# Optimization experiments

Measured on AMD Instinct MI355X. Metric: run time of the kernel, lower is better.

## Reference

```python
import jax, jax.numpy as jnp
import numpy as np

N, C_IN, T, V = 64, 64, 256, 25
C_OUT, S, MAX_N = 256, 3, 500
BN_EPS = 1e-5


def setup_inputs() -> dict:
    key = jax.random.key(0)
    ks = jax.random.split(key, 7)
    x = jax.random.normal(ks[0], (N, C_IN, T, V), dtype=jnp.float32)
    A = jax.random.uniform(ks[1], (S, V, V), dtype=jnp.float32) / V  # fixed adjacency (non-trainable buffer)
    A_pers = jax.random.normal(ks[2], (MAX_N, S, V, V), dtype=jnp.float32) * 1e-3
    # conv_branch_init: std = sqrt(2/(out*1*1*branches))
    conv_w = jax.random.normal(ks[3], (S, C_OUT, C_IN), dtype=jnp.float32) * np.sqrt(2.0 / (C_OUT * S)).astype(np.float32)
    conv_b = jax.random.normal(ks[4], (S, C_OUT), dtype=jnp.float32) * 0.01
    bn_w = jax.random.uniform(ks[5], (C_OUT,), dtype=jnp.float32) + 0.5
    bn_b = jax.random.normal(ks[6], (C_OUT,), dtype=jnp.float32) * 0.01
    return {"x": x, "A": A, "A_pers": A_pers, "conv_w": conv_w,
            "conv_b": conv_b, "bn_w": bn_w, "bn_b": bn_b}


def reference(x, A, A_pers, conv_w, conv_b, bn_w, bn_b):
    n = x.shape[0]  # n <= MAX_N
    A_personalized = jnp.tanh(A_pers[:n])          # (n, S, V, V)
    A_final = A[None] + A_personalized             # (n, S, V, V)
    # Per-sample, per-subset graph aggregation: (C*T, V) @ (V, V)
    xa = jnp.einsum('nctv,nsvw->nsctw', x, A_final)          # (n, S, C, T, V)
    # 1x1 conv per subset, summed over subsets; biases also sum over subsets
    y = jnp.einsum('nsctw,soc->notw', xa, conv_w)
    y = y + jnp.sum(conv_b, axis=0)[None, :, None, None]     # (n, C_OUT, T, V)
    # BatchNorm2d with training=True -> batch statistics (biased variance)
    mean = jnp.mean(y, axis=(0, 2, 3))
    var = jnp.var(y, axis=(0, 2, 3))
    y = (y - mean[None, :, None, None]) * (bn_w / jnp.sqrt(var + BN_EPS))[None, :, None, None] \
        + bn_b[None, :, None, None]
    y = jax.nn.relu(y)
    return (A_personalized, y)
```

## Files before the change

kernel.cpp:

```cpp
#include <hip/hip_runtime.h>
#include <math.h>

#define C_IN   64
#define T_DIM  256
#define V_DIM  25
#define C_OUT  256
#define S_DIM  3
#define BN_EPS 1e-5f

#define SC       (S_DIM * C_IN)
#define TW       (T_DIM * V_DIM)
#define AP_PER_N (S_DIM * V_DIM * V_DIM)
#define LDB      200
#define LDY      204
#define NR       32

#define NBINS    (NR * 2 * C_OUT)
#define NAP      (64 * AP_PER_N)
#define NAFB     (64 * 6 * 64 * 8)
#define NWT      (C_OUT * SC)
#define PREP_TOT (NBINS + NAP + NAFB + NWT)
#define NXU      (64 * 128 * 128 * 16)
#define PREP_ALL (PREP_TOT + NXU)

typedef __attribute__((ext_vector_type(8))) short bf16x8;
typedef __attribute__((ext_vector_type(4))) float f32x4;

__device__ __forceinline__ unsigned short f2bf(float f) {
    unsigned u = __builtin_bit_cast(unsigned, f);
    unsigned r = u + 0x7fffu + ((u >> 16) & 1u);
    return (unsigned short)(r >> 16);
}

__device__ __forceinline__ unsigned pk_bf16(float a, float b) {
    unsigned short ul = __builtin_bit_cast(unsigned short, (__bf16)a);
    unsigned short uh = __builtin_bit_cast(unsigned short, (__bf16)b);
    return (unsigned)ul | ((unsigned)uh << 16);
}

__device__ __forceinline__ void nt_store_f2(float2 v, float* p) {
    __builtin_nontemporal_store(__builtin_bit_cast(double, v), (double*)p);
}

__global__ void k_prep(const float* __restrict__ A, const float* __restrict__ A_pers,
                       const float* __restrict__ conv_w, const float* __restrict__ x,
                       float* __restrict__ bins, float* __restrict__ out_ap,
                       unsigned short* __restrict__ afb, unsigned short* __restrict__ wt_b,
                       unsigned* __restrict__ x_re) {
    int i = blockIdx.x * 256 + threadIdx.x;
    if (i < NBINS) {
        bins[i] = 0.f;
        return;
    }
    i -= NBINS;
    if (i < NAP) {
        out_ap[i] = tanhf(A_pers[i]);
        return;
    }
    i -= NAP;
    if (i < NAFB) {
        int j    = i;
        int k    = j & 7;
        int lane = (j >> 3) & 63;
        int nt   = (j >> 9) & 1;
        int sn   = j >> 10;
        int s    = sn % 3;
        int n    = sn / 3;
        int v    = ((lane >> 4) << 3) + k;
        int w    = nt * 16 + (lane & 15);
        float val = 0.f;
        if (v < V_DIM && w < V_DIM)
            val = A[(s * V_DIM + v) * V_DIM + w] +
                  tanhf(A_pers[((n * S_DIM + s) * V_DIM + v) * V_DIM + w]);
        afb[j] = f2bf(val);
        return;
    }
    i -= NAFB;
    if (i < NWT) {
        int o  = i / SC;
        int sc = i - o * SC;
        int s  = sc >> 6, c = sc & 63;
        wt_b[i] = f2bf(conv_w[(s * C_OUT + o) * C_IN + c]);
        return;
    }
    i -= NWT;
    if (i < NXU) {
        int tile = i >> 11;
        int rem  = i & 2047;
        int row  = rem >> 4;
        int vp   = rem & 15;
        int n = tile >> 7, tp = tile & 127;
        int c = row >> 1, t = row & 1;
        const float* src = x + (size_t)n * (C_IN * TW) + (size_t)c * TW + (2 * tp + t) * V_DIM;
        int v0 = vp * 2;
        unsigned lo = (v0 < V_DIM)     ? f2bf(src[v0])     : 0;
        unsigned hi = (v0 + 1 < V_DIM) ? f2bf(src[v0 + 1]) : 0;
        x_re[i] = lo | (hi << 16);
    }
}

template <int PASS>
__global__ __launch_bounds__(256, 3) void k_gemm(const unsigned short* __restrict__ x_re,
                                                 const unsigned short* __restrict__ afb,
                                                 const unsigned short* __restrict__ wt_b,
                                                 float* __restrict__ y,
                                                 float* __restrict__ bins,
                                                 const float2* __restrict__ ssv) {
    __shared__ __align__(16) char smem[64 * LDY * 4];
    unsigned short* sXa = (unsigned short*)smem;

    const int tid  = threadIdx.x;
    const int tp4  = blockIdx.x;
    const int nIdx = blockIdx.y;
    const int z    = blockIdx.z;
    const int lane = tid & 63;
    const int wv   = tid >> 6;
    const int l15  = lane & 15;
    const int kg   = lane >> 4;
    const int obase = z * 64 + wv * 16;

    bf16x8 aF[6];
    {
        const unsigned short* wrow = wt_b + (size_t)(z * 64 + wv * 16 + l15) * SC + kg * 8;
#pragma unroll
        for (int ks = 0; ks < 6; ++ks)
            aF[ks] = *(const bf16x8*)(wrow + ks * 32);
    }
    bf16x8 bS[6];
    {
        const unsigned short* afbN = afb + (size_t)nIdx * (6 * 64 * 8);
#pragma unroll
        for (int sq = 0; sq < 6; ++sq)
            bS[sq] = *(const bf16x8*)(afbN + (sq * 64 + lane) * 8);
    }
    float2 sh[4];
    if (PASS == 1) {
#pragma unroll
        for (int r = 0; r < 4; ++r)
            sh[r] = ssv[obase + kg * 4 + r];
    }

    for (int j = tid; j < 2800; j += 256) {
        int u = j >= 1400, jj = j - u * 1400;
        ((unsigned*)(sXa + u * 12800))[50 * (LDB / 2) + jj] = 0;
    }

    f32x4 acc[4][4];
#pragma unroll
    for (int q = 0; q < 4; ++q)
#pragma unroll
        for (int nn = 0; nn < 4; ++nn) acc[q][nn] = (f32x4){0.f, 0.f, 0.f, 0.f};

#pragma unroll
    for (int h = 0; h < 2; ++h) {
        bf16x8 aX[2][2];
        {
            const unsigned short* xt0 = x_re + (size_t)(nIdx * 128 + tp4 * 4 + h * 2) * 4096;
#pragma unroll
            for (int u = 0; u < 2; ++u)
#pragma unroll
                for (int m2 = 0; m2 < 2; ++m2)
                    aX[u][m2] = *(const bf16x8*)(xt0 + u * 4096 + ((wv * 2 + m2) * 16 + l15) * 32 + kg * 8);
        }

#pragma unroll
        for (int sq = 0; sq < 6; ++sq) {
            int s = sq >> 1, nt = sq & 1;
            int w = nt * 16 + l15;
#pragma unroll
            for (int u = 0; u < 2; ++u) {
#pragma unroll
                for (int m2 = 0; m2 < 2; ++m2) {
                    int mt = wv * 2 + m2;
                    f32x4 c4 = __builtin_amdgcn_mfma_f32_16x16x32_bf16(
                        aX[u][m2], bS[sq], (f32x4){0.f, 0.f, 0.f, 0.f}, 0, 0, 0);
                    if (w < V_DIM) {
                        unsigned u0 = pk_bf16(c4[0], c4[2]);
                        unsigned u1 = pk_bf16(c4[1], c4[3]);
                        unsigned col = s * 32 + mt * 4 + kg;
                        unsigned* dst = (unsigned*)(sXa + u * 12800);
                        dst[w * (LDB / 2) + col]           = u0;
                        dst[(V_DIM + w) * (LDB / 2) + col] = u1;
                    }
                }
            }
        }
        __syncthreads();

#pragma unroll
        for (int ks = 0; ks < 6; ++ks) {
            bf16x8 bF[2][4];
#pragma unroll
            for (int u = 0; u < 2; ++u)
#pragma unroll
                for (int nn = 0; nn < 4; ++nn)
                    bF[u][nn] = *(const bf16x8*)(sXa + u * 12800 + (nn * 16 + l15) * LDB + ks * 32 + kg * 8);
            __builtin_amdgcn_s_setprio(1);
#pragma unroll
            for (int u = 0; u < 2; ++u)
#pragma unroll
                for (int nn = 0; nn < 4; ++nn)
                    acc[h * 2 + u][nn] = __builtin_amdgcn_mfma_f32_16x16x32_bf16(
                        aF[ks], bF[u][nn], acc[h * 2 + u][nn], 0, 0, 0);
            __builtin_amdgcn_s_setprio(0);
        }
        if (h == 0) __syncthreads();
    }

    if (PASS == 0) {
        const int rep = (blockIdx.y * gridDim.x + blockIdx.x) & (NR - 1);
        float* b0 = bins + rep * 2 * C_OUT;
#pragma unroll
        for (int r = 0; r < 4; ++r) {
            float s1 = 0.f, s2 = 0.f;
#pragma unroll
            for (int q = 0; q < 4; ++q) {
                float v0 = acc[q][0][r], v1 = acc[q][1][r], v2 = acc[q][2][r];
                s1 += v0 + v1 + v2;
                s2 += v0 * v0 + v1 * v1 + v2 * v2;
                if (l15 < 2) {
                    float v3 = acc[q][3][r];
                    s1 += v3;
                    s2 += v3 * v3;
                }
            }
#pragma unroll
            for (int off = 1; off < 16; off <<= 1) {
                s1 += __shfl_xor(s1, off, 64);
                s2 += __shfl_xor(s2, off, 64);
            }
            if (l15 == 0) {
                int o = obase + kg * 4 + r;
                atomicAdd(&b0[o], s1);
                atomicAdd(&b0[C_OUT + o], s2);
            }
        }
    } else {
        __syncthreads();
        float* yS = (float*)smem;
#pragma unroll
        for (int r = 0; r < 4; ++r) {
            int ol = wv * 16 + kg * 4 + r;
            float sc = sh[r].x, sf = sh[r].y;
#pragma unroll
            for (int q = 0; q < 4; ++q) {
                float* sp = yS + ol * LDY + q * 50 + l15;
                sp[0]  = fmaxf(fmaf(acc[q][0][r], sc, sf), 0.f);
                sp[16] = fmaxf(fmaf(acc[q][1][r], sc, sf), 0.f);
                sp[32] = fmaxf(fmaf(acc[q][2][r], sc, sf), 0.f);
                if (l15 < 2)
                    sp[48] = fmaxf(fmaf(acc[q][3][r], sc, sf), 0.f);
            }
        }
        __syncthreads();

        float* ydst = y + ((size_t)nIdx * C_OUT + z * 64) * TW + (size_t)tp4 * 200;
        int o = tid / 100, j2 = tid - o * 100;
#pragma unroll
        for (int k = 0; k < 25; ++k) {
            float2 v = *(const float2*)(yS + o * LDY + 2 * j2);
            nt_store_f2(v, ydst + (size_t)o * TW + 2 * j2);
            o += 2; j2 += 56;
            if (j2 >= 100) { j2 -= 100; ++o; }
        }
    }
}

__global__ void k_stats(const float* __restrict__ bins, const float* __restrict__ bn_w,
                        const float* __restrict__ bn_b, float2* __restrict__ ssv, int n) {
    int o = threadIdx.x;
    float s1 = 0.f, s2 = 0.f;
    for (int rp = 0; rp < NR; ++rp) {
        s1 += bins[rp * 2 * C_OUT + o];
        s2 += bins[rp * 2 * C_OUT + C_OUT + o];
    }
    float cnt   = (float)n * (float)TW;
    float mean  = s1 / cnt;
    float var   = s2 / cnt - mean * mean;
    float scale = bn_w[o] * rsqrtf(var + BN_EPS);
    ssv[o] = make_float2(scale, bn_b[o] - mean * scale);
}

extern "C" void kernel_launch(void* const* d_in, const int* in_sizes, int n_in,
                              void* d_out, int out_size, void* d_ws, size_t ws_size,
                              hipStream_t stream) {
    const float* x      = (const float*)d_in[0];
    const float* A      = (const float*)d_in[1];
    const float* A_pers = (const float*)d_in[2];
    const float* conv_w = (const float*)d_in[3];
    const float* bn_w   = (const float*)d_in[5];
    const float* bn_b   = (const float*)d_in[6];

    const int n = in_sizes[0] / (C_IN * TW);

    float* out_ap = (float*)d_out;
    float* y      = (float*)d_out + (size_t)n * AP_PER_N;

    float*  bins = (float*)d_ws;
    float2* ssv  = (float2*)(bins + NBINS);
    unsigned short* afb  = (unsigned short*)((char*)(ssv + C_OUT));
    unsigned short* wt_b = afb + (size_t)NAFB;
    unsigned short* x_re = wt_b + (size_t)NWT;

    k_prep<<<(PREP_ALL + 255) / 256, 256, 0, stream>>>(A, A_pers, conv_w, x,
                                                       bins, out_ap, afb, wt_b,
                                                       (unsigned*)x_re);

    dim3 grid(T_DIM / 8, n, 4);
    k_gemm<0><<<grid, 256, 0, stream>>>(x_re, afb, wt_b, y, bins, ssv);
    k_stats<<<1, 256, 0, stream>>>(bins, bn_w, bn_b, ssv, n);
    k_gemm<1><<<grid, 256, 0, stream>>>(x_re, afb, wt_b, y, bins, ssv);
}
```

Measured before the change: 277.3 us.

## Split stats pass into z-looped kernel reusing graph-aggregated tile; XCD-swizzle output pass

The statistics pass becomes its own kernel in which each block computes the graph-aggregated x tile once and loops over all four output-channel groups, where before each z-block recomputed the aggregation. The output pass now uses a 1D grid with a block-index remap that keeps the four z-blocks of a tile on the same XCD, aiming for better L2 reuse of x_re. The stats kernel launches four times fewer, larger blocks and holds more accumulators in registers, which may reduce occupancy.

```diff
diff --git a/kernel.cpp b/kernel.cpp
--- a/kernel.cpp
+++ b/kernel.cpp
@@ -99,20 +99,161 @@
     }
 }
 
-template <int PASS>
-__global__ __launch_bounds__(256, 3) void k_gemm(const unsigned short* __restrict__ x_re,
+__global__ __launch_bounds__(256, 3) void k_gsum(const unsigned short* __restrict__ x_re,
                                                  const unsigned short* __restrict__ afb,
                                                  const unsigned short* __restrict__ wt_b,
-                                                 float* __restrict__ y,
-                                                 float* __restrict__ bins,
-                                                 const float2* __restrict__ ssv) {
-    __shared__ __align__(16) char smem[64 * LDY * 4];
-    unsigned short* sXa = (unsigned short*)smem;
+                                                 float* __restrict__ bins) {
+    __shared__ __align__(16) unsigned short sXa[2][64 * LDB];
 
     const int tid  = threadIdx.x;
     const int tp4  = blockIdx.x;
     const int nIdx = blockIdx.y;
-    const int z    = blockIdx.z;
+    const int lane = tid & 63;
+    const int wv   = tid >> 6;
+    const int l15  = lane & 15;
+    const int kg   = lane >> 4;
+
+    bf16x8 bS[6];
+    {
+        const unsigned short* afbN = afb + (size_t)nIdx * (6 * 64 * 8);
+#pragma unroll
+        for (int sq = 0; sq < 6; ++sq)
+            bS[sq] = *(const bf16x8*)(afbN + (sq * 64 + lane) * 8);
+    }
+
+    for (int j = tid; j < 2800; j += 256) {
+        int u = j >= 1400, jj = j - u * 1400;
+        ((unsigned*)sXa[u])[50 * (LDB / 2) + jj] = 0;
+    }
+
+    float s1[4][4], s2[4][4];
+#pragma unroll
+    for (int z = 0; z < 4; ++z)
+#pragma unroll
+        for (int r = 0; r < 4; ++r) { s1[z][r] = 0.f; s2[z][r] = 0.f; }
+
+#pragma unroll
+    for (int h = 0; h < 2; ++h) {
+        bf16x8 aX[2][2];
+        {
+            const unsigned short* xt0 = x_re + (size_t)(nIdx * 128 + tp4 * 4 + h * 2) * 4096;
+#pragma unroll
+            for (int u = 0; u < 2; ++u)
+#pragma unroll
+                for (int m2 = 0; m2 < 2; ++m2)
+                    aX[u][m2] = *(const bf16x8*)(xt0 + u * 4096 + ((wv * 2 + m2) * 16 + l15) * 32 + kg * 8);
+        }
+
+#pragma unroll
+        for (int sq = 0; sq < 6; ++sq) {
+            int s = sq >> 1, nt = sq & 1;
+            int w = nt * 16 + l15;
+#pragma unroll
+            for (int u = 0; u < 2; ++u) {
+#pragma unroll
+                for (int m2 = 0; m2 < 2; ++m2) {
+                    int mt = wv * 2 + m2;
+                    f32x4 c4 = __builtin_amdgcn_mfma_f32_16x16x32_bf16(
+                        aX[u][m2], bS[sq], (f32x4){0.f, 0.f, 0.f, 0.f}, 0, 0, 0);
+                    if (w < V_DIM) {
+                        unsigned u0 = pk_bf16(c4[0], c4[2]);
+                        unsigned u1 = pk_bf16(c4[1], c4[3]);
+                        unsigned col = s * 32 + mt * 4 + kg;
+                        unsigned* dst = (unsigned*)sXa[u];
+                        dst[w * (LDB / 2) + col]           = u0;
+                        dst[(V_DIM + w) * (LDB / 2) + col] = u1;
+                    }
+                }
+            }
+        }
+        __syncthreads();
+
+#pragma unroll
+        for (int z = 0; z < 4; ++z) {
+            bf16x8 aF[6];
+            const unsigned short* wrow = wt_b + (size_t)(z * 64 + wv * 16 + l15) * SC + kg * 8;
+#pragma unroll
+            for (int ks = 0; ks < 6; ++ks)
+                aF[ks] = *(const bf16x8*)(wrow + ks * 32);
+
+            f32x4 acc[2][4];
+#pragma unroll
+            for (int u = 0; u < 2; ++u)
+#pragma unroll
+                for (int nn = 0; nn < 4; ++nn) acc[u][nn] = (f32x4){0.f, 0.f, 0.f, 0.f};
+#pragma unroll
+            for (int ks = 0; ks < 6; ++ks) {
+                bf16x8 bF[2][4];
+#pragma unroll
+                for (int u = 0; u < 2; ++u)
+#pragma unroll
+                    for (int nn = 0; nn < 4; ++nn)
+                        bF[u][nn] = *(const bf16x8*)(sXa[u] + (nn * 16 + l15) * LDB + ks * 32 + kg * 8);
+                __builtin_amdgcn_s_setprio(1);
+#pragma unroll
+                for (int u = 0; u < 2; ++u)
+#pragma unroll
+                    for (int nn = 0; nn < 4; ++nn)
+                        acc[u][nn] = __builtin_amdgcn_mfma_f32_16x16x32_bf16(
+                            aF[ks], bF[u][nn], acc[u][nn], 0, 0, 0);
+                __builtin_amdgcn_s_setprio(0);
+            }
+#pragma unroll
+            for (int r = 0; r < 4; ++r) {
+#pragma unroll
+                for (int u = 0; u < 2; ++u) {
+                    float v0 = acc[u][0][r], v1 = acc[u][1][r], v2 = acc[u][2][r];
+                    s1[z][r] += v0 + v1 + v2;
+                    s2[z][r] += v0 * v0 + v1 * v1 + v2 * v2;
+                    if (l15 < 2) {
+                        float v3 = acc[u][3][r];
+                        s1[z][r] += v3;
+                        s2[z][r] += v3 * v3;
+                    }
+                }
+            }
+        }
+        if (h == 0) __syncthreads();
+    }
+
+    const int rep = (blockIdx.x + blockIdx.y) & (NR - 1);
+    float* b0 = bins + rep * 2 * C_OUT;
+#pragma unroll
+    for (int z = 0; z < 4; ++z) {
+#pragma unroll
+        for (int r = 0; r < 4; ++r) {
+            float a = s1[z][r], b = s2[z][r];
+#pragma unroll
+            for (int off = 1; off < 16; off <<= 1) {
+                a += __shfl_xor(a, off, 64);
+                b += __shfl_xor(b, off, 64);
+            }
+            if (l15 == 0) {
+                int o = z * 64 + wv * 16 + kg * 4 + r;
+                atomicAdd(&b0[o], a);
+                atomicAdd(&b0[C_OUT + o], b);
+            }
+        }
+    }
+}
+
+__global__ __launch_bounds__(256, 3) void k_gy(const unsigned short* __restrict__ x_re,
+                                               const unsigned short* __restrict__ afb,
+                                               const unsigned short* __restrict__ wt_b,
+                                               float* __restrict__ y,
+                                               const float2* __restrict__ ssv) {
+    __shared__ __align__(16) char smem[64 * LDY * 4];
+    unsigned short* sXa = (unsigned short*)smem;
+
+    const int d    = blockIdx.x;
+    const int xcd  = d & 7;
+    const int q8   = d >> 3;
+    const int z    = q8 & 3;
+    const int g    = (q8 >> 2) * 8 + xcd;
+    const int tp4  = g & 31;
+    const int nIdx = g >> 5;
+
+    const int tid  = threadIdx.x;
     const int lane = tid & 63;
     const int wv   = tid >> 6;
     const int l15  = lane & 15;
@@ -134,11 +275,9 @@
             bS[sq] = *(const bf16x8*)(afbN + (sq * 64 + lane) * 8);
     }
     float2 sh[4];
-    if (PASS == 1) {
-#pragma unroll
-        for (int r = 0; r < 4; ++r)
-            sh[r] = ssv[obase + kg * 4 + r];
-    }
+#pragma unroll
+    for (int r = 0; r < 4; ++r)
+        sh[r] = ssv[obase + kg * 4 + r];
 
     for (int j = tid; j < 2800; j += 256) {
         int u = j >= 1400, jj = j - u * 1400;
@@ -147,9 +286,9 @@
 
     f32x4 acc[4][4];
 #pragma unroll
-    for (int q = 0; q < 4; ++q)
-#pragma unroll
-        for (int nn = 0; nn < 4; ++nn) acc[q][nn] = (f32x4){0.f, 0.f, 0.f, 0.f};
+    for (int qq = 0; qq < 4; ++qq)
+#pragma unroll
+        for (int nn = 0; nn < 4; ++nn) acc[qq][nn] = (f32x4){0.f, 0.f, 0.f, 0.f};
 
 #pragma unroll
     for (int h = 0; h < 2; ++h) {
@@ -162,7 +301,6 @@
                 for (int m2 = 0; m2 < 2; ++m2)
                     aX[u][m2] = *(const bf16x8*)(xt0 + u * 4096 + ((wv * 2 + m2) * 16 + l15) * 32 + kg * 8);
         }
-
 #pragma unroll
         for (int sq = 0; sq < 6; ++sq) {
             int s = sq >> 1, nt = sq & 1;
@@ -207,62 +345,32 @@
         if (h == 0) __syncthreads();
     }
 
-    if (PASS == 0) {
-        const int rep = (blockIdx.y * gridDim.x + blockIdx.x) & (NR - 1);
-        float* b0 = bins + rep * 2 * C_OUT;
-#pragma unroll
-        for (int r = 0; r < 4; ++r) {
-            float s1 = 0.f, s2 = 0.f;
-#pragma unroll
-            for (int q = 0; q < 4; ++q) {
-                float v0 = acc[q][0][r], v1 = acc[q][1][r], v2 = acc[q][2][r];
-                s1 += v0 + v1 + v2;
-                s2 += v0 * v0 + v1 * v1 + v2 * v2;
-                if (l15 < 2) {
-                    float v3 = acc[q][3][r];
-                    s1 += v3;
-                    s2 += v3 * v3;
-                }
-            }
-#pragma unroll
-            for (int off = 1; off < 16; off <<= 1) {
-                s1 += __shfl_xor(s1, off, 64);
-                s2 += __shfl_xor(s2, off, 64);
-            }
-            if (l15 == 0) {
-                int o = obase + kg * 4 + r;
-                atomicAdd(&b0[o], s1);
-                atomicAdd(&b0[C_OUT + o], s2);
-            }
-        }
-    } else {
-        __syncthreads();
-        float* yS = (float*)smem;
-#pragma unroll
-        for (int r = 0; r < 4; ++r) {
-            int ol = wv * 16 + kg * 4 + r;
-            float sc = sh[r].x, sf = sh[r].y;
-#pragma unroll
-            for (int q = 0; q < 4; ++q) {
-                float* sp = yS + ol * LDY + q * 50 + l15;
-                sp[0]  = fmaxf(fmaf(acc[q][0][r], sc, sf), 0.f);
-                sp[16] = fmaxf(fmaf(acc[q][1][r], sc, sf), 0.f);
-                sp[32] = fmaxf(fmaf(acc[q][2][r], sc, sf), 0.f);
-                if (l15 < 2)
-                    sp[48] = fmaxf(fmaf(acc[q][3][r], sc, sf), 0.f);
-            }
-        }
-        __syncthreads();
-
-        float* ydst = y + ((size_t)nIdx * C_OUT + z * 64) * TW + (size_t)tp4 * 200;
-        int o = tid / 100, j2 = tid - o * 100;
-#pragma unroll
-        for (int k = 0; k < 25; ++k) {
-            float2 v = *(const float2*)(yS + o * LDY + 2 * j2);
-            nt_store_f2(v, ydst + (size_t)o * TW + 2 * j2);
-            o += 2; j2 += 56;
-            if (j2 >= 100) { j2 -= 100; ++o; }
-        }
+    __syncthreads();
+    float* yS = (float*)smem;
+#pragma unroll
+    for (int r = 0; r < 4; ++r) {
+        int ol = wv * 16 + kg * 4 + r;
+        float sc = sh[r].x, sf = sh[r].y;
+#pragma unroll
+        for (int qq = 0; qq < 4; ++qq) {
+            float* sp = yS + ol * LDY + qq * 50 + l15;
+            sp[0]  = fmaxf(fmaf(acc[qq][0][r], sc, sf), 0.f);
+            sp[16] = fmaxf(fmaf(acc[qq][1][r], sc, sf), 0.f);
+            sp[32] = fmaxf(fmaf(acc[qq][2][r], sc, sf), 0.f);
+            if (l15 < 2)
+                sp[48] = fmaxf(fmaf(acc[qq][3][r], sc, sf), 0.f);
+        }
+    }
+    __syncthreads();
+
+    float* ydst = y + ((size_t)nIdx * C_OUT + z * 64) * TW + (size_t)tp4 * 200;
+    int o = tid / 100, j2 = tid - o * 100;
+#pragma unroll
+    for (int k = 0; k < 25; ++k) {
+        float2 v = *(const float2*)(yS + o * LDY + 2 * j2);
+        nt_store_f2(v, ydst + (size_t)o * TW + 2 * j2);
+        o += 2; j2 += 56;
+        if (j2 >= 100) { j2 -= 100; ++o; }
     }
 }
 
@@ -306,8 +414,7 @@
                                                        bins, out_ap, afb, wt_b,
                                                        (unsigned*)x_re);
 
-    dim3 grid(T_DIM / 8, n, 4);
-    k_gemm<0><<<grid, 256, 0, stream>>>(x_re, afb, wt_b, y, bins, ssv);
+    k_gsum<<<dim3(T_DIM / 8, n), 256, 0, stream>>>(x_re, afb, wt_b, bins);
     k_stats<<<1, 256, 0, stream>>>(bins, bn_w, bn_b, ssv, n);
-    k_gemm<1><<<grid, 256, 0, stream>>>(x_re, afb, wt_b, y, bins, ssv);
-}
+    k_gy<<<dim3(T_DIM / 8 * n * 4), 256, 0, stream>>>(x_re, afb, wt_b, y, ssv);
+}
```

Measured after the change: 379.3 us. +36.8%, slower.
